# Optimization experiments

Measured on AMD Instinct MI355X. Metric: run time of the kernel, lower is better.

The kernel has to match this reference:

```python
import jax, jax.numpy as jnp
import numpy as np

B, T, S, D = 8, 2048, 8, 256


def setup_inputs() -> dict:
    key = jax.random.key(0)
    k1, k2, k3 = jax.random.split(key, 3)
    x = jax.random.normal(k1, (B, T, S, D), dtype=jnp.float32)
    # nn.Linear-style init scale ~ 1/sqrt(fan_in)
    W_in = jax.random.normal(k2, (D, 2 * D), dtype=jnp.float32) / np.sqrt(D)
    b_in = jnp.zeros((2 * D,), dtype=jnp.float32)
    W_out = jax.random.normal(k3, (D, D), dtype=jnp.float32) / np.sqrt(D)
    b_out = jnp.zeros((D,), dtype=jnp.float32)
    return {"x": x, "W_in": W_in, "b_in": b_in, "W_out": W_out, "b_out": b_out}


def reference(x, W_in, b_in, W_out, b_out):
    # in_proj then chunk into gate / candidate (matches torch chunk(2, dim=-1))
    h = jnp.einsum("btsd,de->btse", x, W_in) + b_in  # [B,T,S,2D]
    gate, cand = jnp.split(h, 2, axis=-1)
    alpha = jax.nn.sigmoid(gate)
    cand = jnp.tanh(cand)
    # Diagonal linear recurrence: state_t = a_t * state_{t-1} + b_t
    # with a_t = 1 - alpha_t, b_t = alpha_t * cand_t, state_{-1} = 0.
    a = 1.0 - alpha
    b = alpha * cand

    def combine(c1, c2):
        a1, b1 = c1
        a2, b2 = c2
        return a1 * a2, a2 * b1 + b2

    _, y = jax.lax.associative_scan(combine, (a, b), axis=1)  # [B,T,S,D]
    # dropout is identity in eval mode
    return jnp.einsum("btsd,de->btse", y, W_out) + b_out
```

## Files before the change

kernel.cpp:

```cpp
#include <hip/hip_runtime.h>
#include <hip/hip_bf16.h>
#include <hip/hip_fp16.h>
#include <cstdint>

typedef __attribute__((ext_vector_type(4))) float f32x4;
typedef __attribute__((ext_vector_type(8))) short s16x8;

#define DEVI static __device__ __forceinline__

constexpr int Bc = 8, Tc = 2048, Sc = 8, Dc = 256;
constexpr int Mc = Bc * Tc * Sc;

DEVI unsigned short f2bf(float x) {
  return __bfloat16_as_ushort(__float2bfloat16(x));
}

DEVI f32x4 mfma16(s16x8 a, s16x8 b, f32x4 c) {
  return __builtin_amdgcn_mfma_f32_16x16x32_bf16(a, b, c, 0, 0, 0);
}

DEVI void gld16(const void* g, void* l) {
  __builtin_amdgcn_global_load_lds(
      (const __attribute__((address_space(1))) unsigned int*)g,
      (__attribute__((address_space(3))) unsigned int*)l, 16, 0, 0);
}

__global__ void cvt_x_k(const float* __restrict__ in, unsigned short* __restrict__ out, int n) {
  int i = (blockIdx.x * blockDim.x + threadIdx.x) * 8;
  int stride = gridDim.x * blockDim.x * 8;
  for (; i < n; i += stride) {
    f32x4 a = *(const f32x4*)(in + i);
    f32x4 b = *(const f32x4*)(in + i + 4);
    s16x8 o;
    o[0] = (short)f2bf(a[0]); o[1] = (short)f2bf(a[1]);
    o[2] = (short)f2bf(a[2]); o[3] = (short)f2bf(a[3]);
    o[4] = (short)f2bf(b[0]); o[5] = (short)f2bf(b[1]);
    o[6] = (short)f2bf(b[2]); o[7] = (short)f2bf(b[3]);
    *(s16x8*)(out + i) = o;
  }
}

__global__ void cvtW_k(const float* __restrict__ Win, const float* __restrict__ Wout,
                       unsigned short* __restrict__ wtin, unsigned short* __restrict__ wtout) {
  int tid = blockIdx.x * blockDim.x + threadIdx.x;
  if (tid < 512 * 256) {
    int c = tid >> 8, r = tid & 255;
    wtin[tid] = f2bf(Win[r * 512 + c]);
  } else {
    int t = tid - 512 * 256;
    int c = t >> 8, r = t & 255;
    wtout[t] = f2bf(Wout[r * 256 + c]);
  }
}

__global__ __launch_bounds__(512, 1) void g1scan_k(
    const unsigned short* __restrict__ xb,
    const unsigned short* __restrict__ wt,
    const float* __restrict__ bias,
    unsigned short* __restrict__ yb)
{
  __shared__ unsigned short As[2][8 * 64 * 32];
  __shared__ unsigned short Ws[8 * 128 * 32];
  __shared__ unsigned int   abuf[64 * 64];

  int bid = blockIdx.x;
  int b = bid >> 5, s = (bid >> 2) & 7, dq = bid & 3;
  int tid = threadIdx.x;
  int lane = tid & 63, wave = tid >> 6;
  int rg = wave >> 2, cg = wave & 3;

  const short* xs = (const short*)xb;
  const short* wsrc = (const short*)wt;
  size_t rowbase = (size_t)b * 16384 + s;

  #pragma unroll
  for (int q = 0; q < 8; ++q) {
    int j = q * 512 + tid;
    int p = j >> 9, rem = j & 511, r = rem >> 2, cc = rem & 3;
    int wrow = (r < 64) ? (dq * 64 + r) : (256 + dq * 64 + (r - 64));
    gld16(wsrc + (size_t)wrow * 256 + p * 32 + cc * 8,
          (unsigned short*)Ws + (size_t)j * 8);
  }

  auto STAGE_A = [&](int buf, int t0) {
    #pragma unroll
    for (int q = 0; q < 4; ++q) {
      int j = q * 512 + tid;
      int p = j >> 8, rem = j & 255, r = rem >> 2, cc = rem & 3;
      size_t grow = rowbase + (size_t)(t0 + r) * 8;
      gld16(xs + grow * 256 + p * 32 + cc * 8,
            (unsigned short*)As + (size_t)buf * 16384 + (size_t)j * 8);
    }
  };

  STAGE_A(0, 0);

  int cl = cg * 16 + (lane & 15);
  float bg = bias[dq * 64 + cl];
  float bc = bias[256 + dq * 64 + cl];
  int kg = (lane >> 4) * 8;

  float stt = 0.f;

  __syncthreads();

  for (int ch = 0; ch < 32; ++ch) {
    int cur = ch & 1;
    if (ch < 31) STAGE_A(cur ^ 1, (ch + 1) * 64);

    f32x4 accG[2] = {}, accC[2] = {};
    #pragma unroll
    for (int kf = 0; kf < 8; ++kf) {
      s16x8 aF[2], bG, bC;
      #pragma unroll
      for (int mf = 0; mf < 2; ++mf)
        aF[mf] = *(const s16x8*)((unsigned short*)As + (size_t)cur * 16384 + kf * 2048 +
                                 (rg * 32 + mf * 16 + (lane & 15)) * 32 + kg);
      bG = *(const s16x8*)((unsigned short*)Ws + kf * 4096 + cl * 32 + kg);
      bC = *(const s16x8*)((unsigned short*)Ws + kf * 4096 + (64 + cl) * 32 + kg);
      #pragma unroll
      for (int mf = 0; mf < 2; ++mf) {
        accG[mf] = mfma16(aF[mf], bG, accG[mf]);
        accC[mf] = mfma16(aF[mf], bC, accC[mf]);
      }
    }

    unsigned pk[2][4];
    #pragma unroll
    for (int mf = 0; mf < 2; ++mf)
      #pragma unroll
      for (int r = 0; r < 4; ++r) {
        float g = accG[mf][r] + bg;
        float c = accC[mf][r] + bc;
        float alpha = 1.f / (1.f + __expf(-g));
        float e2 = __expf(2.f * c);
        float th = 1.f - 2.f / (e2 + 1.f);
        __half2 h;
        h.x = __float2half(1.f - alpha);
        h.y = __float2half(alpha * th);
        pk[mf][r] = *(unsigned*)&h;
      }

    __syncthreads();

    #pragma unroll
    for (int mf = 0; mf < 2; ++mf)
      #pragma unroll
      for (int r = 0; r < 4; ++r) {
        int row = rg * 32 + mf * 16 + (lane >> 4) * 4 + r;
        abuf[row * 64 + cl] = pk[mf][r];
      }

    __syncthreads();

    if (wave == 0) {
      size_t ybase = (rowbase + (size_t)ch * 64 * 8) * 256 + dq * 64 + lane;
      #pragma unroll
      for (int j0 = 0; j0 < 64; j0 += 16) {
        unsigned uu[16];
        #pragma unroll
        for (int u = 0; u < 16; ++u) uu[u] = abuf[(j0 + u) * 64 + lane];
        #pragma unroll
        for (int u = 0; u < 16; ++u) {
          __half2 h = *(__half2*)&uu[u];
          stt = fmaf(__half2float(h.x), stt, __half2float(h.y));
          yb[ybase + (size_t)(j0 + u) * 8 * 256] = f2bf(stt);
        }
      }
    }
  }
}

__global__ __launch_bounds__(256, 2) void gemm2_k(
    const unsigned short* __restrict__ yb,
    const unsigned short* __restrict__ wt,
    const float* __restrict__ bias,
    float* __restrict__ out)
{
  __shared__ unsigned short As[2][2][128 * 32];
  __shared__ unsigned short Bs[2][2][128 * 32];

  int bid = blockIdx.x;
  int swz = (bid & 7) * 256 + (bid >> 3);
  int mtile = swz >> 1, ctile = swz & 1;
  int tid = threadIdx.x;
  int lane = tid & 63, wave = tid >> 6;
  int wr = wave >> 1, wc = wave & 1;

  const short* ys = (const short*)yb;
  const short* wsrc = (const short*)wt;

  auto STAGE = [&](int buf, int k0) {
    unsigned short* Ad = &As[buf][0][0];
    unsigned short* Bd = &Bs[buf][0][0];
    #pragma unroll
    for (int q = 0; q < 4; ++q) {
      int j = q * 256 + tid;
      int p = j >> 9, r = (j >> 2) & 127, cc = j & 3;
      int koff = k0 + p * 32 + cc * 8;
      gld16(ys + (size_t)(mtile * 128 + r) * 256 + koff, Ad + (size_t)j * 8);
      gld16(wsrc + (size_t)(ctile * 128 + r) * 256 + koff, Bd + (size_t)j * 8);
    }
  };

  f32x4 acc[4][4] = {};

  STAGE(0, 0);
  __syncthreads();
  #pragma unroll
  for (int kk = 0; kk < 4; ++kk) {
    int cur = kk & 1;
    if (kk < 3) STAGE(cur ^ 1, (kk + 1) * 64);
    int kg = (lane >> 4) * 8;
    #pragma unroll
    for (int ks = 0; ks < 2; ++ks) {
      s16x8 aF[4], bF[4];
      #pragma unroll
      for (int mf = 0; mf < 4; ++mf)
        aF[mf] = *(const s16x8*)&As[cur][ks][(wr * 64 + mf * 16 + (lane & 15)) * 32 + kg];
      #pragma unroll
      for (int nf = 0; nf < 4; ++nf)
        bF[nf] = *(const s16x8*)&Bs[cur][ks][(wc * 64 + nf * 16 + (lane & 15)) * 32 + kg];
      #pragma unroll
      for (int mf = 0; mf < 4; ++mf)
        #pragma unroll
        for (int nf = 0; nf < 4; ++nf)
          acc[mf][nf] = mfma16(aF[mf], bF[nf], acc[mf][nf]);
    }
    if (kk < 3) __syncthreads();
  }

  int orow0 = mtile * 128 + wr * 64 + (lane >> 4) * 4;
  #pragma unroll
  for (int nf = 0; nf < 4; ++nf) {
    int col = ctile * 128 + wc * 64 + nf * 16 + (lane & 15);
    float bo = bias[col];
    #pragma unroll
    for (int mf = 0; mf < 4; ++mf) {
      #pragma unroll
      for (int r = 0; r < 4; ++r) {
        int row = orow0 + mf * 16 + r;
        out[(size_t)row * 256 + col] = acc[mf][nf][r] + bo;
      }
    }
  }
}

extern "C" void kernel_launch(void* const* d_in, const int* in_sizes, int n_in,
                              void* d_out, int out_size, void* d_ws, size_t ws_size,
                              hipStream_t stream)
{
  const float* x    = (const float*)d_in[0];
  const float* Win  = (const float*)d_in[1];
  const float* bin  = (const float*)d_in[2];
  const float* Wout = (const float*)d_in[3];
  const float* bout = (const float*)d_in[4];
  float* out = (float*)d_out;
  char* ws = (char*)d_ws;

  unsigned short* wtin  = (unsigned short*)(ws);
  unsigned short* wtout = (unsigned short*)(ws + 262144);
  unsigned short* yb    = (unsigned short*)(ws + 393216);
  unsigned short* xb    = (unsigned short*)(ws + 393216 + (size_t)Mc * 256 * 2);

  cvt_x_k<<<1024, 256, 0, stream>>>(x, xb, Mc * 256);
  cvtW_k<<<768, 256, 0, stream>>>(Win, Wout, wtin, wtout);
  g1scan_k<<<256, 512, 0, stream>>>(xb, wtin, bin, yb);
  gemm2_k<<<2048, 256, 0, stream>>>(yb, wtout, bout, out);
}
```

Baseline: 186.9 us.

## Parallelize per-chunk recurrence across all eight waves with segmented scan

The sequential 64-step scan over each chunk previously ran only in wave 0, leaving the other seven waves idle. Now each wave reduces an 8-step segment to an (A,B) pair. It writes the pair to shared memory, then every wave recomputes the carry-in across the 8 segments and emits its own 8 outputs. This shortens the serial critical path per chunk, at the cost of an extra barrier and a small amount of redundant carry computation.

```diff
diff --git a/kernel.cpp b/kernel.cpp
--- a/kernel.cpp
+++ b/kernel.cpp
@@ -62,6 +62,7 @@
   __shared__ unsigned short As[2][8 * 64 * 32];
   __shared__ unsigned short Ws[8 * 128 * 32];
   __shared__ unsigned int   abuf[64 * 64];
+  __shared__ float segA[8][64], segB[8][64];
 
   int bid = blockIdx.x;
   int b = bid >> 5, s = (bid >> 2) & 7, dq = bid & 3;
@@ -153,20 +154,36 @@
 
     __syncthreads();
 
-    if (wave == 0) {
-      size_t ybase = (rowbase + (size_t)ch * 64 * 8) * 256 + dq * 64 + lane;
-      #pragma unroll
-      for (int j0 = 0; j0 < 64; j0 += 16) {
-        unsigned uu[16];
-        #pragma unroll
-        for (int u = 0; u < 16; ++u) uu[u] = abuf[(j0 + u) * 64 + lane];
-        #pragma unroll
-        for (int u = 0; u < 16; ++u) {
-          __half2 h = *(__half2*)&uu[u];
-          stt = fmaf(__half2float(h.x), stt, __half2float(h.y));
-          yb[ybase + (size_t)(j0 + u) * 8 * 256] = f2bf(stt);
-        }
-      }
+    float av[8], bv[8];
+    float A = 1.f, Bv = 0.f;
+    #pragma unroll
+    for (int u = 0; u < 8; ++u) {
+      unsigned vv = abuf[(wave * 8 + u) * 64 + lane];
+      __half2 h = *(__half2*)&vv;
+      av[u] = __half2float(h.x);
+      bv[u] = __half2float(h.y);
+      A = av[u] * A;
+      Bv = fmaf(av[u], Bv, bv[u]);
+    }
+    segA[wave][lane] = A;
+    segB[wave][lane] = Bv;
+
+    __syncthreads();
+
+    float sin = stt, s_w = stt;
+    #pragma unroll
+    for (int w2 = 0; w2 < 8; ++w2) {
+      if (w2 == wave) s_w = sin;
+      sin = fmaf(segA[w2][lane], sin, segB[w2][lane]);
+    }
+    stt = sin;
+
+    size_t ybase = (rowbase + (size_t)(ch * 64 + wave * 8) * 8) * 256 + dq * 64 + lane;
+    float sv = s_w;
+    #pragma unroll
+    for (int u = 0; u < 8; ++u) {
+      sv = fmaf(av[u], sv, bv[u]);
+      yb[ybase + (size_t)u * 8 * 256] = f2bf(sv);
     }
   }
 }
```

Measured after the change: 190.5 us. No clear change (+1.9%).
